# Kernel optimization log

Hardware: AMD Instinct MI355X
Metric: run time of the kernel (lower is better)

The kernel has to match this reference:

```python
import jax, jax.numpy as jnp
import numpy as np

N_NODES = 50000
N_EDGES = 800000
IN_DIM = 256
HID = 128
OUT = 128
LEAKY_SLOPE = 0.01


def setup_inputs() -> dict:
    key = jax.random.key(0)
    ks = jax.random.split(key, 12)
    s = 0.05
    return {
        "h": jax.random.normal(ks[0], (N_NODES, IN_DIM), dtype=jnp.float32),
        "src": jax.random.randint(ks[1], (N_EDGES,), 0, N_NODES, dtype=jnp.int32),
        "dst": jax.random.randint(ks[2], (N_EDGES,), 0, N_NODES, dtype=jnp.int32),
        "W1": jax.random.normal(ks[3], (HID, IN_DIM), dtype=jnp.float32) * s,
        "b1": jax.random.normal(ks[4], (HID,), dtype=jnp.float32) * s,
        "a1": jax.random.normal(ks[5], (2 * HID,), dtype=jnp.float32) * s,
        "ab1": jax.random.normal(ks[6], (), dtype=jnp.float32) * s,
        "W2": jax.random.normal(ks[7], (OUT, HID), dtype=jnp.float32) * s,
        "b2": jax.random.normal(ks[8], (OUT,), dtype=jnp.float32) * s,
        "a2": jax.random.normal(ks[9], (2 * OUT,), dtype=jnp.float32) * s,
        "ab2": jax.random.normal(ks[10], (), dtype=jnp.float32) * s,
    }


def gat_layer(h, src, dst, W, b, a, ab, n_nodes):
    # z = fc(h)
    z = h @ W.T + b                      # [N, D]
    D = z.shape[-1]
    zs = z[src]                           # [E, D] gather src features
    zd = z[dst]                           # [E, D] gather dst features
    # attn_fc(cat[zs, zd]) == zs @ a[:D] + zd @ a[D:] + ab
    e = zs @ a[:D] + zd @ a[D:] + ab      # [E]
    e = jnp.where(e > 0, e, LEAKY_SLOPE * e)  # leaky_relu, slope 0.01
    # segment softmax over edges grouped by destination node
    m = jax.ops.segment_max(e, dst, num_segments=n_nodes)   # [N]
    ex = jnp.exp(e - m[dst])                                  # [E]
    denom = jax.ops.segment_sum(ex, dst, num_segments=n_nodes)  # [N]
    alpha = ex / denom[dst]                                   # [E]
    # weighted scatter-sum of src features into dst nodes
    return jax.ops.segment_sum(alpha[:, None] * zs, dst, num_segments=n_nodes)


def reference(h, src, dst, W1, b1, a1, ab1, W2, b2, a2, ab2):
    n = h.shape[0]
    h1 = jax.nn.elu(gat_layer(h, src, dst, W1, b1, a1, ab1, n))
    h2 = jax.nn.elu(gat_layer(h1, src, dst, W2, b2, a2, ab2, n))
    return h2
```

## Files before the change

kernel.cpp:

```cpp
#include <hip/hip_runtime.h>
#include <hip/hip_bf16.h>

#define N_NODES 50000
#define N_EDGES 800000
#define IN_DIM  256
#define HID     128
#define LEAKY   0.01f

#define EDGE_BLOCKS  ((N_EDGES + 255) / 256)
#define NODE_WBLKS   (N_NODES / 4)
#define SCAN_BLOCKS  ((N_NODES + 255) / 256)
#define W1_ELEMS  (HID * IN_DIM)
#define W2_ELEMS  (HID * HID)

#define TM        64
#define FC_BLOCKS ((N_NODES + TM - 1) / TM)

typedef __attribute__((ext_vector_type(8))) short short8;
typedef __attribute__((ext_vector_type(4))) float f32x4;

#define GLDS(g, l)                                                              \
    __builtin_amdgcn_global_load_lds(                                           \
        (const __attribute__((address_space(1))) void*)(g),                     \
        (__attribute__((address_space(3))) void*)(l), 16, 0, 0)

__device__ __forceinline__ unsigned short f2bf(float x) {
    union { __hip_bfloat16 b; unsigned short u; } c;
    c.b = __float2bfloat16(x);
    return c.u;
}
__device__ __forceinline__ float bf2f(unsigned short u) {
    union { unsigned int u; float f; } c;
    c.u = ((unsigned int)u) << 16;
    return c.f;
}
__device__ __forceinline__ float2 bfu2(unsigned int u) {
    float2 r;
    r.x = bf2f((unsigned short)(u & 0xffff));
    r.y = bf2f((unsigned short)(u >> 16));
    return r;
}
__device__ __forceinline__ float lky(float x) { return x > 0.f ? x : LEAKY * x; }
__device__ __forceinline__ float rl_f(float v, int l) {
    return __int_as_float(__builtin_amdgcn_readlane(__float_as_int(v), l));
}

__device__ __forceinline__ void cvt8(const float4 v0, const float4 v1,
                                     short8& hi, short8& lo) {
    float f[8] = {v0.x, v0.y, v0.z, v0.w, v1.x, v1.y, v1.z, v1.w};
#pragma unroll
    for (int j = 0; j < 8; j++) {
        unsigned short h = f2bf(f[j]);
        hi[j] = (short)h;
        lo[j] = (short)f2bf(f[j] - bf2f(h));
    }
}


__global__ void hist_split(const int* __restrict__ dst, int* __restrict__ counts,
                           int* __restrict__ erank,
                           const float* __restrict__ W1, unsigned short* __restrict__ w1hi,
                           unsigned short* __restrict__ w1lo,
                           const float* __restrict__ W2, unsigned short* __restrict__ w2hi,
                           unsigned short* __restrict__ w2lo) {
    int i = blockIdx.x * 256 + threadIdx.x;
    if (i < N_EDGES) erank[i] = atomicAdd(&counts[dst[i]], 1);
    if (i < W1_ELEMS) {
        float x = W1[i];
        unsigned short h = f2bf(x);
        w1hi[i] = h;
        w1lo[i] = f2bf(x - bf2f(h));
    } else if (i < W1_ELEMS + W2_ELEMS) {
        int j = i - W1_ELEMS;
        float x = W2[j];
        unsigned short h = f2bf(x);
        w2hi[j] = h;
        w2lo[j] = f2bf(x - bf2f(h));
    }
}

__global__ void scan_block(const int* __restrict__ counts, int* __restrict__ offsets,
                           int* __restrict__ bsums) {
    __shared__ int sh[256];
    int tid = threadIdx.x;
    int i = blockIdx.x * 256 + tid;
    int v = (i < N_NODES) ? counts[i] : 0;
    sh[tid] = v;
    __syncthreads();
    for (int o = 1; o < 256; o <<= 1) {
        int t = (tid >= o) ? sh[tid - o] : 0;
        __syncthreads();
        sh[tid] += t;
        __syncthreads();
    }
    if (i < N_NODES) offsets[i] = sh[tid] - v;
    if (tid == 255) bsums[blockIdx.x] = sh[255];
}

__global__ void scan_add(int* __restrict__ offsets, const int* __restrict__ bsums) {
    __shared__ int sh[256];
    int tid = threadIdx.x;
    int b = blockIdx.x;
    sh[tid] = (tid < b) ? bsums[tid] : 0;
    __syncthreads();
    for (int o = 128; o > 0; o >>= 1) {
        if (tid < o) sh[tid] += sh[tid + o];
        __syncthreads();
    }
    int base = sh[0];
    int i = b * 256 + tid;
    if (i < N_NODES) offsets[i] += base;
    if (i == N_NODES) offsets[N_NODES] = N_EDGES;
}

__global__ void fill_kernel(const int* __restrict__ dst, const int* __restrict__ src,
                            const int* __restrict__ erank,
                            const int* __restrict__ offsets,
                            int* __restrict__ csr_src) {
    int i = blockIdx.x * 256 + threadIdx.x;
    if (i < N_EDGES) {
        int d = dst[i];
        int slot = offsets[d] + erank[i];
        __builtin_nontemporal_store(src[i], &csr_src[slot]);
    }
}


__device__ __forceinline__ void epi(const f32x4* accn, int lrow0, int m0, int q, int lane,
                                    const float* __restrict__ bias,
                                    const float* __restrict__ attn,
                                    unsigned short* __restrict__ Zb,
                                    float* __restrict__ sbuf) {
    int r = lane & 15;
    int lrowbase = lrow0 + (lane >> 4) * 4;
    float ps[4] = {0.f, 0.f, 0.f, 0.f};
    float pd[4] = {0.f, 0.f, 0.f, 0.f};
#pragma unroll
    for (int nt = 0; nt < 4; nt++) {
        int n = q * 64 + nt * 16 + r;
        float bn = bias[n];
        float aS = attn[n];
        float aD = attn[HID + n];
#pragma unroll
        for (int reg = 0; reg < 4; reg++) {
            float zv = accn[nt][reg] + bn;
            if (m0 + lrowbase + reg < N_NODES)
                Zb[(size_t)(m0 + lrowbase + reg) * HID + n] = f2bf(zv);
            ps[reg] += zv * aS;
            pd[reg] += zv * aD;
        }
    }
#pragma unroll
    for (int o = 1; o < 16; o <<= 1) {
#pragma unroll
        for (int reg = 0; reg < 4; reg++) {
            ps[reg] += __shfl_xor(ps[reg], o, 64);
            pd[reg] += __shfl_xor(pd[reg], o, 64);
        }
    }
    if (r == 0) {
#pragma unroll
        for (int reg = 0; reg < 4; reg++) {
            sbuf[q * 128 + lrowbase + reg] = ps[reg];
            sbuf[q * 128 + 64 + lrowbase + reg] = pd[reg];
        }
    }
}

__device__ __forceinline__ void score_combine(const float* __restrict__ sbuf, int tid, int m0,
                                              float* __restrict__ sS, float* __restrict__ sD) {
    if (tid < TM) {
        int gr = m0 + tid;
        if (gr < N_NODES) {
            sS[gr] = sbuf[tid] + sbuf[128 + tid];
            sD[gr] = sbuf[64 + tid] + sbuf[128 + 64 + tid];
        }
    }
}


__launch_bounds__(256)
__global__ void gemm_fc1(const float* __restrict__ A,
                         const unsigned short* __restrict__ Whi,
                         const unsigned short* __restrict__ Wlo,
                         const float* __restrict__ bias,
                         const float* __restrict__ attn,
                         unsigned short* __restrict__ Zb,
                         float* __restrict__ sS, float* __restrict__ sD) {
    __shared__ char lds[2][24576];

    int tid  = threadIdx.x;
    int lane = tid & 63;
    int w    = tid >> 6;
    int q    = w & 1;
    int mh   = w >> 1;
    int m0   = blockIdx.x * TM;
    int r    = lane & 15;
    int kg   = lane >> 4;

    const char* gp[6];
    int gstep[6];
    int loff[6];
#pragma unroll
    for (int j = 0; j < 6; j++) {
        int c = w * 6 + j;
        loff[j] = c * 1024;
        if (c < 8) {
            int S = c >> 1, hh = c & 1;
            int row = m0 + S * 16 + r;
            if (row >= N_NODES) row = N_NODES - 1;
            gp[j] = (const char*)(A + (size_t)row * IN_DIM + kg * 8 + hh * 4);
            gstep[j] = 32 * 4;
        } else if (c < 16) {
            int nt = c - 8;
            gp[j] = (const char*)(Whi + (size_t)(nt * 16 + r) * IN_DIM + kg * 8);
            gstep[j] = 32 * 2;
        } else {
            int nt = c - 16;
            gp[j] = (const char*)(Wlo + (size_t)(nt * 16 + r) * IN_DIM + kg * 8);
            gstep[j] = 32 * 2;
        }
    }

#define STAGE1(b)                                                   \
    {                                                               \
        _Pragma("unroll") for (int j = 0; j < 6; j++) {             \
            GLDS(gp[j], lds[b] + loff[j]);                          \
            gp[j] += gstep[j];                                      \
        }                                                           \
    }

    f32x4 acc[2][4];
#pragma unroll
    for (int s = 0; s < 2; s++)
#pragma unroll
        for (int nt = 0; nt < 4; nt++) acc[s][nt] = (f32x4){0.f, 0.f, 0.f, 0.f};

    STAGE1(0);
    __syncthreads();

#pragma unroll
    for (int kt = 0; kt < IN_DIM / 32; kt++) {
        const int cur = kt & 1;
        if (kt < IN_DIM / 32 - 1) STAGE1(cur ^ 1);

        const float* Af = (const float*)lds[cur];
        const unsigned short* Bh = (const unsigned short*)(lds[cur] + 8192);
        const unsigned short* Bl = (const unsigned short*)(lds[cur] + 16384);

        short8 ah[2], al[2], bh[4], bl[4];
#pragma unroll
        for (int s = 0; s < 2; s++) {
            int S = mh * 2 + s;
            float4 v0 = *(const float4*)(Af + (S * 2 + 0) * 256 + lane * 4);
            float4 v1 = *(const float4*)(Af + (S * 2 + 1) * 256 + lane * 4);
            cvt8(v0, v1, ah[s], al[s]);
        }
#pragma unroll
        for (int nt = 0; nt < 4; nt++) {
            bh[nt] = *(const short8*)(Bh + (q * 4 + nt) * 512 + lane * 8);
            bl[nt] = *(const short8*)(Bl + (q * 4 + nt) * 512 + lane * 8);
        }
#pragma unroll
        for (int s = 0; s < 2; s++)
#pragma unroll
            for (int nt = 0; nt < 4; nt++) {
                acc[s][nt] = __builtin_amdgcn_mfma_f32_16x16x32_bf16(ah[s], bh[nt], acc[s][nt], 0, 0, 0);
                acc[s][nt] = __builtin_amdgcn_mfma_f32_16x16x32_bf16(al[s], bh[nt], acc[s][nt], 0, 0, 0);
                acc[s][nt] = __builtin_amdgcn_mfma_f32_16x16x32_bf16(ah[s], bl[nt], acc[s][nt], 0, 0, 0);
            }
        __syncthreads();
    }
#undef STAGE1

    float* sbuf = (float*)lds[0];
#pragma unroll
    for (int s = 0; s < 2; s++)
        epi(acc[s], mh * 32 + s * 16, m0, q, lane, bias, attn, Zb, sbuf);
    __syncthreads();
    score_combine(sbuf, tid, m0, sS, sD);
}


__launch_bounds__(256)
__global__ void gemm_fc2(const unsigned short* __restrict__ Abf,
                         const unsigned short* __restrict__ Whi,
                         const unsigned short* __restrict__ Wlo,
                         const float* __restrict__ bias,
                         const float* __restrict__ attn,
                         unsigned short* __restrict__ Zb,
                         float* __restrict__ sS, float* __restrict__ sD) {
    __shared__ char lds[2][20480];

    int tid  = threadIdx.x;
    int lane = tid & 63;
    int w    = tid >> 6;
    int q    = w & 1;
    int mh   = w >> 1;
    int m0   = blockIdx.x * TM;
    int r    = lane & 15;
    int kg   = lane >> 4;

    const char* gp[5];
    int loff[5];
#pragma unroll
    for (int j = 0; j < 5; j++) {
        int c = w * 5 + j;
        loff[j] = c * 1024;
        if (c < 4) {
            int row = m0 + c * 16 + r;
            if (row >= N_NODES) row = N_NODES - 1;
            gp[j] = (const char*)(Abf + (size_t)row * HID + kg * 8);
        } else if (c < 12) {
            gp[j] = (const char*)(Whi + (size_t)((c - 4) * 16 + r) * HID + kg * 8);
        } else {
            gp[j] = (const char*)(Wlo + (size_t)((c - 12) * 16 + r) * HID + kg * 8);
        }
    }

#define STAGE2(b)                                                   \
    {                                                               \
        _Pragma("unroll") for (int j = 0; j < 5; j++) {             \
            GLDS(gp[j], lds[b] + loff[j]);                          \
            gp[j] += 64;                                            \
        }                                                           \
    }

    f32x4 acc[2][4];
#pragma unroll
    for (int s = 0; s < 2; s++)
#pragma unroll
        for (int nt = 0; nt < 4; nt++) acc[s][nt] = (f32x4){0.f, 0.f, 0.f, 0.f};

    STAGE2(0);
    __syncthreads();

#pragma unroll
    for (int kt = 0; kt < HID / 32; kt++) {
        const int cur = kt & 1;
        if (kt < HID / 32 - 1) STAGE2(cur ^ 1);

        const unsigned short* Aq = (const unsigned short*)lds[cur];
        const unsigned short* Bh = (const unsigned short*)(lds[cur] + 4096);
        const unsigned short* Bl = (const unsigned short*)(lds[cur] + 12288);

        short8 a8[2], bh[4], bl[4];
#pragma unroll
        for (int s = 0; s < 2; s++)
            a8[s] = *(const short8*)(Aq + (mh * 2 + s) * 512 + lane * 8);
#pragma unroll
        for (int nt = 0; nt < 4; nt++) {
            bh[nt] = *(const short8*)(Bh + (q * 4 + nt) * 512 + lane * 8);
            bl[nt] = *(const short8*)(Bl + (q * 4 + nt) * 512 + lane * 8);
        }
#pragma unroll
        for (int s = 0; s < 2; s++)
#pragma unroll
            for (int nt = 0; nt < 4; nt++) {
                acc[s][nt] = __builtin_amdgcn_mfma_f32_16x16x32_bf16(a8[s], bh[nt], acc[s][nt], 0, 0, 0);
                acc[s][nt] = __builtin_amdgcn_mfma_f32_16x16x32_bf16(a8[s], bl[nt], acc[s][nt], 0, 0, 0);
            }
        __syncthreads();
    }
#undef STAGE2

    float* sbuf = (float*)lds[0];
#pragma unroll
    for (int s = 0; s < 2; s++)
        epi(acc[s], mh * 32 + s * 16, m0, q, lane, bias, attn, Zb, sbuf);
    __syncthreads();
    score_combine(sbuf, tid, m0, sS, sD);
}


template <int OUT_BF>
__launch_bounds__(256)
__global__ void aggregate(const unsigned short* __restrict__ Zb,
                          const int* __restrict__ csr_src,
                          const int* __restrict__ offsets,
                          const float* __restrict__ sS,
                          const float* __restrict__ sD,
                          const float* __restrict__ ab,
                          unsigned short* __restrict__ OutBf,
                          float* __restrict__ OutF) {
    int v = blockIdx.x * 4 + (threadIdx.x >> 6);
    int lane = threadIdx.x & 63;
    int off = offsets[v];
    int deg = offsets[v + 1] - off;
    float sdv = sD[v] + ab[0];

    const unsigned int* Zrow = (const unsigned int*)Zb;
    float2 acc = {0.f, 0.f};

    if (deg <= 64) {
        bool act = lane < deg;
        int s_l = 0;
        float x = -3.0e38f;
        if (act) {
            s_l = csr_src[off + lane];
            x = lky(sS[s_l] + sdv);
        }
        float mx = x;
#pragma unroll
        for (int o = 32; o > 0; o >>= 1) mx = fmaxf(mx, __shfl_xor(mx, o, 64));
        float ex = act ? __expf(x - mx) : 0.f;
        float sum = ex;
#pragma unroll
        for (int o = 32; o > 0; o >>= 1) sum += __shfl_xor(sum, o, 64);
        float al_l = (deg > 0) ? ex / sum : 0.f;

        int t = 0;
        for (; t + 16 <= deg; t += 16) {
            int   s[16];
            float a[16];
            unsigned int rw[16];
#pragma unroll
            for (int j = 0; j < 16; j++) {
                s[j] = __builtin_amdgcn_readlane(s_l, t + j);
                a[j] = rl_f(al_l, t + j);
            }
#pragma unroll
            for (int j = 0; j < 16; j++)
                rw[j] = Zrow[(size_t)s[j] * (HID / 2) + lane];
#pragma unroll
            for (int j = 0; j < 16; j++) {
                float2 zz = bfu2(rw[j]);
                acc.x += a[j] * zz.x;
                acc.y += a[j] * zz.y;
            }
        }
        for (; t + 4 <= deg; t += 4) {
            int   s[4];
            float a[4];
            unsigned int rw[4];
#pragma unroll
            for (int j = 0; j < 4; j++) {
                s[j] = __builtin_amdgcn_readlane(s_l, t + j);
                a[j] = rl_f(al_l, t + j);
            }
#pragma unroll
            for (int j = 0; j < 4; j++)
                rw[j] = Zrow[(size_t)s[j] * (HID / 2) + lane];
#pragma unroll
            for (int j = 0; j < 4; j++) {
                float2 zz = bfu2(rw[j]);
                acc.x += a[j] * zz.x;
                acc.y += a[j] * zz.y;
            }
        }
        for (; t < deg; t++) {
            int sj = __builtin_amdgcn_readlane(s_l, t);
            float aj = rl_f(al_l, t);
            float2 zz = bfu2(Zrow[(size_t)sj * (HID / 2) + lane]);
            acc.x += aj * zz.x;
            acc.y += aj * zz.y;
        }
    } else {
        float mx = -3.0e38f;
        for (int t = lane; t < deg; t += 64) {
            int s = csr_src[off + t];
            mx = fmaxf(mx, lky(sS[s] + sdv));
        }
#pragma unroll
        for (int o = 32; o > 0; o >>= 1) mx = fmaxf(mx, __shfl_xor(mx, o, 64));
        float sum = 0.f;
        for (int t = lane; t < deg; t += 64) {
            int s = csr_src[off + t];
            sum += __expf(lky(sS[s] + sdv) - mx);
        }
#pragma unroll
        for (int o = 32; o > 0; o >>= 1) sum += __shfl_xor(sum, o, 64);
        float inv = 1.f / sum;
        for (int t = 0; t < deg; t++) {
            int s = csr_src[off + t];
            float al = __expf(lky(sS[s] + sdv) - mx) * inv;
            float2 zz = bfu2(Zrow[(size_t)s * (HID / 2) + lane]);
            acc.x += al * zz.x;
            acc.y += al * zz.y;
        }
    }

    acc.x = acc.x > 0.f ? acc.x : __expf(acc.x) - 1.f;
    acc.y = acc.y > 0.f ? acc.y : __expf(acc.y) - 1.f;

    if (OUT_BF) {
        ushort2 o2;
        o2.x = f2bf(acc.x);
        o2.y = f2bf(acc.y);
        *((ushort2*)(OutBf + (size_t)v * HID + lane * 2)) = o2;
    } else {
        float2 o2 = {acc.x, acc.y};
        *((float2*)(OutF + (size_t)v * HID + lane * 2)) = o2;
    }
}


extern "C" void kernel_launch(void* const* d_in, const int* in_sizes, int n_in,
                              void* d_out, int out_size, void* d_ws, size_t ws_size,
                              hipStream_t stream) {
    const float* h   = (const float*)d_in[0];
    const int*   src = (const int*)d_in[1];
    const int*   dst = (const int*)d_in[2];
    const float* W1  = (const float*)d_in[3];
    const float* b1  = (const float*)d_in[4];
    const float* a1  = (const float*)d_in[5];
    const float* ab1 = (const float*)d_in[6];
    const float* W2  = (const float*)d_in[7];
    const float* b2  = (const float*)d_in[8];
    const float* a2  = (const float*)d_in[9];
    const float* ab2 = (const float*)d_in[10];
    float* out = (float*)d_out;

    unsigned short* zb = (unsigned short*)d_ws;
    float* sS = (float*)(zb + (size_t)N_NODES * HID);
    float* sD = sS + N_NODES;
    int* counts  = (int*)(sD + N_NODES);
    int* offsets = counts + N_NODES;
    int* bsums   = offsets + N_NODES + 16;
    unsigned short* h1   = (unsigned short*)(bsums + 256);
    unsigned short* w1hi = h1 + (size_t)N_NODES * HID;
    unsigned short* w1lo = w1hi + W1_ELEMS;
    unsigned short* w2hi = w1lo + W1_ELEMS;
    unsigned short* w2lo = w2hi + W2_ELEMS;
    int* csr_src = (int*)(w2lo + W2_ELEMS);
    int* erank   = csr_src + N_EDGES;

    hipMemsetAsync(counts, 0, (size_t)N_NODES * sizeof(int), stream);

    hist_split<<<EDGE_BLOCKS, 256, 0, stream>>>(dst, counts, erank,
                                                W1, w1hi, w1lo, W2, w2hi, w2lo);
    scan_block<<<SCAN_BLOCKS, 256, 0, stream>>>(counts, offsets, bsums);
    scan_add<<<SCAN_BLOCKS, 256, 0, stream>>>(offsets, bsums);
    fill_kernel<<<EDGE_BLOCKS, 256, 0, stream>>>(dst, src, erank, offsets, csr_src);

    gemm_fc1<<<FC_BLOCKS, 256, 0, stream>>>(h, w1hi, w1lo, b1, a1, zb, sS, sD);
    aggregate<1><<<NODE_WBLKS, 256, 0, stream>>>(zb, csr_src, offsets, sS, sD, ab1, h1, nullptr);

    gemm_fc2<<<FC_BLOCKS, 256, 0, stream>>>(h1, w2hi, w2lo, b2, a2, zb, sS, sD);
    aggregate<0><<<NODE_WBLKS, 256, 0, stream>>>(zb, csr_src, offsets, sS, sD, ab2, nullptr, out);
}
```

Before: 287.6 us.

## Triple-buffer LDS staging in both FC GEMMs with manual vmcnt waits

```diff
diff --git a/kernel.cpp b/kernel.cpp
--- a/kernel.cpp
+++ b/kernel.cpp
@@ -187,7 +187,7 @@
                          const float* __restrict__ attn,
                          unsigned short* __restrict__ Zb,
                          float* __restrict__ sS, float* __restrict__ sD) {
-    __shared__ char lds[2][24576];
+    __shared__ char lds[3][24576];
 
     int tid  = threadIdx.x;
     int lane = tid & 63;
@@ -236,17 +236,25 @@
 #pragma unroll
         for (int nt = 0; nt < 4; nt++) acc[s][nt] = (f32x4){0.f, 0.f, 0.f, 0.f};
 
+    const int NT = IN_DIM / 32;
     STAGE1(0);
-    __syncthreads();
-
-#pragma unroll
-    for (int kt = 0; kt < IN_DIM / 32; kt++) {
-        const int cur = kt & 1;
-        if (kt < IN_DIM / 32 - 1) STAGE1(cur ^ 1);
-
-        const float* Af = (const float*)lds[cur];
-        const unsigned short* Bh = (const unsigned short*)(lds[cur] + 8192);
-        const unsigned short* Bl = (const unsigned short*)(lds[cur] + 16384);
+    STAGE1(1);
+
+#pragma unroll
+    for (int kt = 0; kt < NT; kt++) {
+        const int cb = kt % 3;
+        if (kt < NT - 1) {
+            asm volatile("s_waitcnt vmcnt(6)" ::: "memory");
+        } else {
+            asm volatile("s_waitcnt vmcnt(0)" ::: "memory");
+        }
+        __builtin_amdgcn_s_barrier();
+        __builtin_amdgcn_sched_barrier(0);
+        if (kt + 2 < NT) STAGE1((kt + 2) % 3);
+
+        const float* Af = (const float*)lds[cb];
+        const unsigned short* Bh = (const unsigned short*)(lds[cb] + 8192);
+        const unsigned short* Bl = (const unsigned short*)(lds[cb] + 16384);
 
         short8 ah[2], al[2], bh[4], bl[4];
 #pragma unroll
@@ -269,7 +277,6 @@
                 acc[s][nt] = __builtin_amdgcn_mfma_f32_16x16x32_bf16(al[s], bh[nt], acc[s][nt], 0, 0, 0);
                 acc[s][nt] = __builtin_amdgcn_mfma_f32_16x16x32_bf16(ah[s], bl[nt], acc[s][nt], 0, 0, 0);
             }
-        __syncthreads();
     }
 #undef STAGE1
 
@@ -290,7 +297,7 @@
                          const float* __restrict__ attn,
                          unsigned short* __restrict__ Zb,
                          float* __restrict__ sS, float* __restrict__ sD) {
-    __shared__ char lds[2][20480];
+    __shared__ char lds[3][20480];
 
     int tid  = threadIdx.x;
     int lane = tid & 63;
@@ -332,17 +339,25 @@
 #pragma unroll
         for (int nt = 0; nt < 4; nt++) acc[s][nt] = (f32x4){0.f, 0.f, 0.f, 0.f};
 
+    const int NT = HID / 32;
     STAGE2(0);
-    __syncthreads();
-
-#pragma unroll
-    for (int kt = 0; kt < HID / 32; kt++) {
-        const int cur = kt & 1;
-        if (kt < HID / 32 - 1) STAGE2(cur ^ 1);
-
-        const unsigned short* Aq = (const unsigned short*)lds[cur];
-        const unsigned short* Bh = (const unsigned short*)(lds[cur] + 4096);
-        const unsigned short* Bl = (const unsigned short*)(lds[cur] + 12288);
+    STAGE2(1);
+
+#pragma unroll
+    for (int kt = 0; kt < NT; kt++) {
+        const int cb = kt % 3;
+        if (kt < NT - 1) {
+            asm volatile("s_waitcnt vmcnt(5)" ::: "memory");
+        } else {
+            asm volatile("s_waitcnt vmcnt(0)" ::: "memory");
+        }
+        __builtin_amdgcn_s_barrier();
+        __builtin_amdgcn_sched_barrier(0);
+        if (kt + 2 < NT) STAGE2((kt + 2) % 3);
+
+        const unsigned short* Aq = (const unsigned short*)lds[cb];
+        const unsigned short* Bh = (const unsigned short*)(lds[cb] + 4096);
+        const unsigned short* Bl = (const unsigned short*)(lds[cb] + 12288);
 
         short8 a8[2], bh[4], bl[4];
 #pragma unroll
@@ -360,11 +375,10 @@
                 acc[s][nt] = __builtin_amdgcn_mfma_f32_16x16x32_bf16(a8[s], bh[nt], acc[s][nt], 0, 0, 0);
                 acc[s][nt] = __builtin_amdgcn_mfma_f32_16x16x32_bf16(a8[s], bl[nt], acc[s][nt], 0, 0, 0);
             }
-        __syncthreads();
     }
 #undef STAGE2
 
-    float* sbuf = (float*)lds[0];
+    float* sbuf = (float*)lds[1];
 #pragma unroll
     for (int s = 0; s < 2; s++)
         epi(acc[s], mh * 32 + s * 16, m0, q, lane, bias, attn, Zb, sbuf);
```

After: 291.8 us. Within noise of the previous version (+1.4%).
